# Kernel tuning notes

Measured on AMD Instinct MI355X. Metric: run time of the kernel, lower is better.

## Reference

```python
import jax, jax.numpy as jnp
import numpy as np

N_NODES = 2176
N_IN = 64
N_HID = 2048
N_OUT = 64
NODE_DIM = 64
HEADS = 4


def _build_edge_index():
    hs, os_ = N_IN, N_IN + N_HID
    # input -> hidden block (order: for i: for h)
    s1 = np.repeat(np.arange(0, N_IN), N_HID)
    t1 = np.tile(np.arange(hs, os_), N_IN)
    # hidden -> output block (order: for h: for o)
    s2 = np.repeat(np.arange(hs, os_), N_OUT)
    t2 = np.tile(np.arange(os_, N_NODES), N_HID)
    return jnp.asarray(np.stack([np.concatenate([s1, s2]), np.concatenate([t1, t2])]), dtype=jnp.int32)


def setup_inputs() -> dict:
    key = jax.random.key(0)
    ks = jax.random.split(key, 20)
    D, H = NODE_DIM, HEADS
    edge_index = _build_edge_index()  # [2, E]
    E = edge_index.shape[1]

    def xavier(k, shape):
        fan_in, fan_out = shape[0], shape[1]
        lim = float(np.sqrt(6.0 / (fan_in + fan_out)))
        return jax.random.uniform(k, shape, jnp.float32, -lim, lim)

    return {
        "x_input": jax.random.normal(ks[0], (N_IN,), jnp.float32),
        "node_features": jax.random.normal(ks[1], (N_NODES, D), jnp.float32) * 0.1,
        "edge_weights": jax.random.normal(ks[2], (E, 1), jnp.float32) * 0.1,
        "edge_index": edge_index,
        "wq1": xavier(ks[3], (D, D * H)), "wk1": xavier(ks[4], (D, D * H)),
        "wv1": xavier(ks[5], (D, D * H)), "we1": xavier(ks[6], (1, H)),
        "wo1": xavier(ks[7], (D * H, D)), "bo1": jnp.zeros((D,), jnp.float32),
        "wq2": xavier(ks[8], (D, D * H)), "wk2": xavier(ks[9], (D, D * H)),
        "wv2": xavier(ks[10], (D, D * H)), "we2": xavier(ks[11], (1, H)),
        "wo2": xavier(ks[12], (D * H, D)), "bo2": jnp.zeros((D,), jnp.float32),
        "wproj": xavier(ks[13], (D, 1)), "bproj": jnp.zeros((1,), jnp.float32),
        "num_output_nodes": N_OUT,
    }


def _message_pass(x, edge_index, ew, wq, wk, wv, we, wo, bo):
    # x: [N, D_in]; edge_index: [2, E]; ew: [E, 1]
    src, tgt = edge_index[0], edge_index[1]
    dout = wo.shape[1]
    heads = wq.shape[1] // dout
    q = (x[tgt] @ wq).reshape(-1, heads, dout)  # [E, H, D]
    k = (x[src] @ wk).reshape(-1, heads, dout)
    v = (x[src] @ wv).reshape(-1, heads, dout)
    attn = (q * k).sum(-1) / jnp.sqrt(jnp.float32(dout)) + ew @ we  # [E, H]
    # NOTE: the per-target segment-softmax in the torch source is dead code;
    # the effective math is leaky_relu then a global softmax over edges.
    attn = jax.nn.leaky_relu(attn, negative_slope=0.2)
    attn = jax.nn.softmax(attn, axis=0)
    weighted_v = (attn[:, :, None] * v).reshape(-1, heads * dout)  # [E, H*D]
    out = jax.ops.segment_sum(weighted_v, tgt, num_segments=x.shape[0])  # [N, H*D]
    out = out @ wo + bo
    return out + x  # residual (in_channels == out_channels)


def reference(x_input, node_features, edge_weights, edge_index,
              wq1, wk1, wv1, we1, wo1, bo1,
              wq2, wk2, wv2, we2, wo2, bo2,
              wproj, bproj, num_output_nodes):
    n_in = x_input.shape[0]
    x = node_features.at[:n_in, 0].set(x_input)
    x = jax.nn.relu(_message_pass(x, edge_index, edge_weights, wq1, wk1, wv1, we1, wo1, bo1))
    x = jax.nn.relu(_message_pass(x, edge_index, edge_weights, wq2, wk2, wv2, we2, wo2, bo2))
    out_nodes = x[x.shape[0] - num_output_nodes:]
    output = jax.nn.sigmoid(out_nodes @ wproj + bproj).squeeze()
    return output, x
```

## Files before the change

### kernel.cpp

```cpp
#include <hip/hip_runtime.h>
#include <math.h>

#define E1 131072

__device__ __forceinline__ void gemm_nn_acc(const float* __restrict__ A,
                                            const float* __restrict__ B,
                                            float acc[4][4], int tr, int tc) {
  for (int k4 = 0; k4 < 16; ++k4) {
    float4 b0 = *(const float4*)&B[(k4 * 4 + 0) * 68 + tc * 4];
    float4 b1 = *(const float4*)&B[(k4 * 4 + 1) * 68 + tc * 4];
    float4 b2 = *(const float4*)&B[(k4 * 4 + 2) * 68 + tc * 4];
    float4 b3 = *(const float4*)&B[(k4 * 4 + 3) * 68 + tc * 4];
#pragma unroll
    for (int a = 0; a < 4; ++a) {
      float4 av = *(const float4*)&A[(tr + 16 * a) * 68 + k4 * 4];
      acc[a][0] += av.x * b0.x + av.y * b1.x + av.z * b2.x + av.w * b3.x;
      acc[a][1] += av.x * b0.y + av.y * b1.y + av.z * b2.y + av.w * b3.y;
      acc[a][2] += av.x * b0.z + av.y * b1.z + av.z * b2.z + av.w * b3.z;
      acc[a][3] += av.x * b0.w + av.y * b1.w + av.z * b2.w + av.w * b3.w;
    }
  }
}

__device__ __forceinline__ void gemm_nt_acc(const float* __restrict__ A,
                                            const float* __restrict__ B,
                                            float acc[4][4], int tr, int tc) {
  for (int k4 = 0; k4 < 16; ++k4) {
    float4 av[4], bv[4];
#pragma unroll
    for (int a = 0; a < 4; ++a) av[a] = *(const float4*)&A[(tr + 16 * a) * 68 + k4 * 4];
#pragma unroll
    for (int b = 0; b < 4; ++b) bv[b] = *(const float4*)&B[(tc + 16 * b) * 68 + k4 * 4];
#pragma unroll
    for (int a = 0; a < 4; ++a)
#pragma unroll
      for (int b = 0; b < 4; ++b)
        acc[a][b] += av[a].x * bv[b].x + av[a].y * bv[b].y +
                     av[a].z * bv[b].z + av[a].w * bv[b].w;
  }
}

__device__ __forceinline__ void st_tile(float* __restrict__ C, const float acc[4][4],
                                        int tr, int tc) {
#pragma unroll
  for (int a = 0; a < 4; ++a)
    *(float4*)&C[(tr + 16 * a) * 68 + tc * 4] =
        make_float4(acc[a][0], acc[a][1], acc[a][2], acc[a][3]);
}

__device__ __forceinline__ void ld_x(float* __restrict__ dst, const float* __restrict__ src,
                                     int tid, bool sub, const float* __restrict__ xinp) {
  for (int t4 = tid; t4 < 1024; t4 += 256) {
    int r = t4 >> 4, c0 = (t4 & 15) * 4;
    float4 v = *(const float4*)(src + t4 * 4);
    if (sub && c0 == 0) v.x = xinp[r];
    *(float4*)&dst[r * 68 + c0] = v;
  }
}

__global__ __launch_bounds__(256) void k_mm(const float* __restrict__ wq1, const float* __restrict__ wk1,
                                            const float* __restrict__ wv1, const float* __restrict__ wo1,
                                            const float* __restrict__ wq2, const float* __restrict__ wk2,
                                            const float* __restrict__ wv2, const float* __restrict__ wo2,
                                            float* __restrict__ Mb, float* __restrict__ W2b) {
  __shared__ float A[64 * 68];
  __shared__ float B[64 * 68];
  const int bid = blockIdx.x, tid = threadIdx.x;
  const int L = bid >> 3, type = (bid >> 2) & 1, h = bid & 3;
  const float* wq = L ? wq2 : wq1;
  const float* wk = L ? wk2 : wk1;
  const float* wv = L ? wv2 : wv1;
  const float* wo = L ? wo2 : wo1;
  const int tr = tid >> 4, tc = tid & 15;
  float acc[4][4];
#pragma unroll
  for (int a = 0; a < 4; ++a)
#pragma unroll
    for (int q = 0; q < 4; ++q) acc[a][q] = 0.f;

  if (type == 0) {
    for (int t4 = tid; t4 < 1024; t4 += 256) {
      int r = t4 >> 4, c0 = (t4 & 15) * 4;
      *(float4*)&A[r * 68 + c0] = *(const float4*)(wq + r * 256 + h * 64 + c0);
      *(float4*)&B[r * 68 + c0] = *(const float4*)(wk + r * 256 + h * 64 + c0);
    }
    __syncthreads();
    gemm_nt_acc(A, B, acc, tr, tc);
    float* out = Mb + L * 16384 + h * 4096;
#pragma unroll
    for (int a = 0; a < 4; ++a)
#pragma unroll
      for (int b = 0; b < 4; ++b)
        out[(tr + 16 * a) * 64 + tc + 16 * b] = acc[a][b];
  } else {
    for (int t4 = tid; t4 < 1024; t4 += 256) {
      int r = t4 >> 4, c0 = (t4 & 15) * 4;
      *(float4*)&A[r * 68 + c0] = *(const float4*)(wv + r * 256 + h * 64 + c0);
      *(float4*)&B[r * 68 + c0] = *(const float4*)(wo + (h * 64 + r) * 64 + c0);
    }
    __syncthreads();
    gemm_nn_acc(A, B, acc, tr, tc);
    float* out = W2b + L * 16384;
#pragma unroll
    for (int a = 0; a < 4; ++a)
      *(float4*)&out[(h * 64 + tr + 16 * a) * 64 + tc * 4] =
          make_float4(acc[a][0], acc[a][1], acc[a][2], acc[a][3]);
  }
}

template<bool SUB>
__global__ __launch_bounds__(256) void k_attn(const float* __restrict__ x,
                                              const float* __restrict__ xinp,
                                              const float* __restrict__ Mb,
                                              const float* __restrict__ we,
                                              const float* __restrict__ ew,
                                              float* __restrict__ AggH,
                                              float* __restrict__ part,
                                              float* __restrict__ bsum) {
  __shared__ float A[64 * 68];
  __shared__ float B[64 * 68];
  __shared__ float C[64 * 68];
  __shared__ float D[64 * 68];
  __shared__ float Em[64 * 68];
  __shared__ float wred[4];
  const int bid = blockIdx.x, tid = threadIdx.x;
  const bool r1 = bid < 128;
  const int tile = (r1 ? bid : bid - 128) >> 2;
  const int h = bid & 3;
  const int j0 = tile * 64;
  const int rowSrc = r1 ? 0 : (64 + j0);
  const int rowQ = r1 ? (64 + j0) : 2112;
  const int tr = tid >> 4, tc = tid & 15;
  const float weh = we[h];
  const float* Mh = Mb + h * 4096;

  ld_x(A, x + rowSrc * 64, tid, SUB && r1, xinp);
  ld_x(B, x + rowQ * 64, tid, false, nullptr);
  for (int t4 = tid; t4 < 1024; t4 += 256) {
    int r = t4 >> 4, c0 = (t4 & 15) * 4;
    *(float4*)&Em[r * 68 + c0] = *(const float4*)(Mh + r * 64 + c0);
  }
  if (r1) {
    for (int t4 = tid; t4 < 1024; t4 += 256) {
      int i = t4 >> 4, jl0 = (t4 & 15) * 4;
      *(float4*)&D[i * 68 + jl0] = *(const float4*)(ew + i * 2048 + j0 + jl0);
    }
  } else {
    for (int t4 = tid; t4 < 1024; t4 += 256) {
      int jl = t4 >> 4, o0 = (t4 & 15) * 4;
      *(float4*)&D[jl * 68 + o0] = *(const float4*)(ew + E1 + (j0 + jl) * 64 + o0);
    }
  }
  __syncthreads();

  {
    float t_[4][4];
#pragma unroll
    for (int a = 0; a < 4; ++a)
#pragma unroll
      for (int q = 0; q < 4; ++q) t_[a][q] = 0.f;
    gemm_nn_acc(B, Em, t_, tr, tc);
    st_tile(C, t_, tr, tc);
  }
  __syncthreads();

  float acc[4][4];
#pragma unroll
  for (int a = 0; a < 4; ++a)
#pragma unroll
    for (int b = 0; b < 4; ++b) acc[a][b] = 0.f;
  gemm_nt_acc(C, A, acc, tr, tc);
  float esum = 0.f;
#pragma unroll
  for (int a = 0; a < 4; ++a) {
    int row = tr + 16 * a;
#pragma unroll
    for (int b = 0; b < 4; ++b) {
      int col = tc + 16 * b;
      float v = acc[a][b] * 0.125f + D[col * 68 + row] * weh;
      v = (v >= 0.f) ? v : 0.2f * v;
      v = fminf(v, 60.f);
      float e = __expf(v);
      esum += e;
      B[row * 68 + col] = e;
    }
  }
#pragma unroll
  for (int s = 1; s < 64; s <<= 1) esum += __shfl_xor(esum, s);
  if ((tid & 63) == 0) wred[tid >> 6] = esum;
  __syncthreads();

  float u[4][4];
#pragma unroll
  for (int a = 0; a < 4; ++a)
#pragma unroll
    for (int q = 0; q < 4; ++q) u[a][q] = 0.f;
  gemm_nn_acc(B, A, u, tr, tc);
  if (r1) {
#pragma unroll
    for (int a = 0; a < 4; ++a)
      *(float4*)&AggH[(j0 + tr + 16 * a) * 256 + h * 64 + tc * 4] =
          make_float4(u[a][0], u[a][1], u[a][2], u[a][3]);
  } else {
#pragma unroll
    for (int a = 0; a < 4; ++a)
      *(float4*)&part[tile * 16384 + (tr + 16 * a) * 256 + h * 64 + tc * 4] =
          make_float4(u[a][0], u[a][1], u[a][2], u[a][3]);
  }
  if (tid == 0) bsum[bid] = (wred[0] + wred[1]) + (wred[2] + wred[3]);
}

template<bool SUB, bool HEAD>
__global__ __launch_bounds__(256) void k_proj(const float* __restrict__ xin,
                                              const float* __restrict__ xinp,
                                              const float* __restrict__ AggH,
                                              const float* __restrict__ part,
                                              const float* __restrict__ bsum,
                                              const float* __restrict__ W2,
                                              const float* __restrict__ bo,
                                              const float* __restrict__ wproj,
                                              const float* __restrict__ bproj,
                                              float* __restrict__ xout,
                                              float* __restrict__ outh) {
  __shared__ float As[4][260];
  const int bid = blockIdx.x, tid = threadIdx.x;
  const int n0 = bid * 4;
  const int nl = tid >> 6, d = tid & 63;
  const int node = n0 + nl;

  float inv[4];
  {
    int l = tid & 63;
#pragma unroll
    for (int hh = 0; hh < 4; ++hh) {
      float s = (l < 32) ? bsum[l * 4 + hh] : bsum[128 + (l - 32) * 4 + hh];
#pragma unroll
      for (int st = 1; st < 64; st <<= 1) s += __shfl_xor(s, st);
      inv[hh] = 1.f / s;
    }
  }

  float xres = xin[node * 64 + d];
  if (SUB) {
    if (d == 0 && node < 64) xres = xinp[node];
  }

  float val;
  if (n0 < 64) {
    val = xres + bo[d];
  } else {
    if (n0 < 2112) {
      int a = tid >> 6, c0 = (tid & 63) * 4;
      float4 v = *(const float4*)&AggH[(n0 - 64 + a) * 256 + c0];
      float iv = inv[c0 >> 6];
      *(float4*)&As[a][c0] = make_float4(v.x * iv, v.y * iv, v.z * iv, v.w * iv);
    } else {
      int a = tid >> 6, c0 = (tid & 63) * 4;
      float4 s = make_float4(0.f, 0.f, 0.f, 0.f);
      for (int ch = 0; ch < 32; ++ch) {
        float4 v = *(const float4*)&part[ch * 16384 + (n0 - 2112 + a) * 256 + c0];
        s.x += v.x; s.y += v.y; s.z += v.z; s.w += v.w;
      }
      float iv = inv[c0 >> 6];
      *(float4*)&As[a][c0] = make_float4(s.x * iv, s.y * iv, s.z * iv, s.w * iv);
    }
    __syncthreads();
    float acc = xres + bo[d];
    for (int c4 = 0; c4 < 64; ++c4) {
      float4 a4 = *(const float4*)&As[nl][c4 * 4];
      acc += a4.x * W2[(c4 * 4 + 0) * 64 + d] + a4.y * W2[(c4 * 4 + 1) * 64 + d] +
             a4.z * W2[(c4 * 4 + 2) * 64 + d] + a4.w * W2[(c4 * 4 + 3) * 64 + d];
    }
    val = acc;
  }
  val = fmaxf(val, 0.f);
  xout[node * 64 + d] = val;

  if (HEAD) {
    if (n0 >= 2112) {
      float wv = val * wproj[d];
#pragma unroll
      for (int st = 1; st < 64; st <<= 1) wv += __shfl_xor(wv, st);
      if ((tid & 63) == 0) outh[node - 2112] = 1.f / (1.f + __expf(-(wv + bproj[0])));
    }
  }
}

extern "C" void kernel_launch(void* const* d_in, const int* in_sizes, int n_in,
                              void* d_out, int out_size, void* d_ws, size_t ws_size,
                              hipStream_t stream) {
  const float* x_input       = (const float*)d_in[0];
  const float* node_features = (const float*)d_in[1];
  const float* edge_weights  = (const float*)d_in[2];
  const float* wq1 = (const float*)d_in[4];
  const float* wk1 = (const float*)d_in[5];
  const float* wv1 = (const float*)d_in[6];
  const float* we1 = (const float*)d_in[7];
  const float* wo1 = (const float*)d_in[8];
  const float* bo1 = (const float*)d_in[9];
  const float* wq2 = (const float*)d_in[10];
  const float* wk2 = (const float*)d_in[11];
  const float* wv2 = (const float*)d_in[12];
  const float* we2 = (const float*)d_in[13];
  const float* wo2 = (const float*)d_in[14];
  const float* bo2 = (const float*)d_in[15];
  const float* wproj = (const float*)d_in[16];
  const float* bproj = (const float*)d_in[17];

  float* out = (float*)d_out;
  float* ws = (float*)d_ws;
  float* xB   = ws;
  float* AggH = xB + 139264;
  float* part = AggH + 524288;
  float* bsum = part + 524288;
  float* Mb   = bsum + 256;
  float* W2b  = Mb + 32768;

  k_mm<<<16, 256, 0, stream>>>(wq1, wk1, wv1, wo1, wq2, wk2, wv2, wo2, Mb, W2b);

  k_attn<true><<<256, 256, 0, stream>>>(node_features, x_input, Mb, we1,
                                        edge_weights, AggH, part, bsum);
  k_proj<true, false><<<544, 256, 0, stream>>>(node_features, x_input, AggH, part, bsum,
                                               W2b, bo1, nullptr, nullptr, xB, nullptr);

  k_attn<false><<<256, 256, 0, stream>>>(xB, nullptr, Mb + 16384, we2,
                                         edge_weights, AggH, part, bsum);
  k_proj<false, true><<<544, 256, 0, stream>>>(xB, nullptr, AggH, part, bsum,
                                               W2b + 16384, bo2, wproj, bproj, out + 64, out);
}
```

Baseline: 57.57 us.

## Fold weight-product kernel into first attention kernel, dropping a launch

Removes the separate k_mm launch. The first attention kernel now computes K=x·Wk and Q=x·Wq per head directly instead of using a precomputed Wq·Wk^T matrix. Its first 12 blocks also compute the layer-2 Wq·Wk^T products and both layers' Wv·Wo products for later kernels. This saves a launch and a serial dependency, but adds two extra 64x64 GEMMs per block in layer 1, raises shared memory per block to seven tiles (which may lower occupancy), and gives a few blocks a longer tail.

```diff
diff --git a/kernel.cpp b/kernel.cpp
--- a/kernel.cpp
+++ b/kernel.cpp
@@ -58,70 +58,186 @@
   }
 }
 
-__global__ __launch_bounds__(256) void k_mm(const float* __restrict__ wq1, const float* __restrict__ wk1,
-                                            const float* __restrict__ wv1, const float* __restrict__ wo1,
-                                            const float* __restrict__ wq2, const float* __restrict__ wk2,
-                                            const float* __restrict__ wv2, const float* __restrict__ wo2,
-                                            float* __restrict__ Mb, float* __restrict__ W2b) {
-  __shared__ float A[64 * 68];
-  __shared__ float B[64 * 68];
+__device__ __forceinline__ void ld_w(float* __restrict__ dst, const float* __restrict__ w,
+                                     int h, int tid) {
+  for (int t4 = tid; t4 < 1024; t4 += 256) {
+    int k = t4 >> 4, c0 = (t4 & 15) * 4;
+    *(float4*)&dst[k * 68 + c0] = *(const float4*)(w + k * 256 + h * 64 + c0);
+  }
+}
+
+__global__ __launch_bounds__(256) void k_attn1(const float* __restrict__ x,
+                                               const float* __restrict__ xinp,
+                                               const float* __restrict__ wq1,
+                                               const float* __restrict__ wk1,
+                                               const float* __restrict__ we1,
+                                               const float* __restrict__ ew,
+                                               const float* __restrict__ wq2,
+                                               const float* __restrict__ wk2,
+                                               const float* __restrict__ wv1,
+                                               const float* __restrict__ wo1,
+                                               const float* __restrict__ wv2,
+                                               const float* __restrict__ wo2,
+                                               float* __restrict__ AggH,
+                                               float* __restrict__ part,
+                                               float* __restrict__ bsum,
+                                               float* __restrict__ Mb,
+                                               float* __restrict__ W2b) {
+  __shared__ float A[4352];
+  __shared__ float B[4352];
+  __shared__ float C[4352];
+  __shared__ float D[4352];
+  __shared__ float Ew[4352];
+  __shared__ float F[4352];
+  __shared__ float G[4352];
+  __shared__ float wred[4];
   const int bid = blockIdx.x, tid = threadIdx.x;
-  const int L = bid >> 3, type = (bid >> 2) & 1, h = bid & 3;
-  const float* wq = L ? wq2 : wq1;
-  const float* wk = L ? wk2 : wk1;
-  const float* wv = L ? wv2 : wv1;
-  const float* wo = L ? wo2 : wo1;
+  const bool r1 = bid < 128;
+  const int tile = (r1 ? bid : bid - 128) >> 2;
+  const int h = bid & 3;
+  const int j0 = tile * 64;
+  const int rowSrc = r1 ? 0 : (64 + j0);
+  const int rowQ = r1 ? (64 + j0) : 2112;
   const int tr = tid >> 4, tc = tid & 15;
-  float acc[4][4];
-#pragma unroll
-  for (int a = 0; a < 4; ++a)
-#pragma unroll
-    for (int q = 0; q < 4; ++q) acc[a][q] = 0.f;
-
-  if (type == 0) {
+  const float weh = we1[h];
+
+  ld_x(A, x + rowSrc * 64, tid, r1, xinp);
+  ld_x(B, x + rowQ * 64, tid, false, nullptr);
+  ld_w(Ew, wk1, h, tid);
+  ld_w(F, wq1, h, tid);
+  if (r1) {
     for (int t4 = tid; t4 < 1024; t4 += 256) {
-      int r = t4 >> 4, c0 = (t4 & 15) * 4;
-      *(float4*)&A[r * 68 + c0] = *(const float4*)(wq + r * 256 + h * 64 + c0);
-      *(float4*)&B[r * 68 + c0] = *(const float4*)(wk + r * 256 + h * 64 + c0);
-    }
-    __syncthreads();
-    gemm_nt_acc(A, B, acc, tr, tc);
-    float* out = Mb + L * 16384 + h * 4096;
-#pragma unroll
-    for (int a = 0; a < 4; ++a)
-#pragma unroll
-      for (int b = 0; b < 4; ++b)
-        out[(tr + 16 * a) * 64 + tc + 16 * b] = acc[a][b];
+      int i = t4 >> 4, jl0 = (t4 & 15) * 4;
+      *(float4*)&G[i * 68 + jl0] = *(const float4*)(ew + i * 2048 + j0 + jl0);
+    }
   } else {
     for (int t4 = tid; t4 < 1024; t4 += 256) {
-      int r = t4 >> 4, c0 = (t4 & 15) * 4;
-      *(float4*)&A[r * 68 + c0] = *(const float4*)(wv + r * 256 + h * 64 + c0);
-      *(float4*)&B[r * 68 + c0] = *(const float4*)(wo + (h * 64 + r) * 64 + c0);
-    }
+      int jl = t4 >> 4, o0 = (t4 & 15) * 4;
+      *(float4*)&G[jl * 68 + o0] = *(const float4*)(ew + E1 + (j0 + jl) * 64 + o0);
+    }
+  }
+  __syncthreads();
+
+  {
+    float kt[4][4];
+#pragma unroll
+    for (int a = 0; a < 4; ++a)
+#pragma unroll
+      for (int q = 0; q < 4; ++q) kt[a][q] = 0.f;
+    gemm_nn_acc(A, Ew, kt, tr, tc);
+    st_tile(C, kt, tr, tc);
+    float qt[4][4];
+#pragma unroll
+    for (int a = 0; a < 4; ++a)
+#pragma unroll
+      for (int q = 0; q < 4; ++q) qt[a][q] = 0.f;
+    gemm_nn_acc(B, F, qt, tr, tc);
+    st_tile(D, qt, tr, tc);
+  }
+  __syncthreads();
+
+  float acc[4][4];
+#pragma unroll
+  for (int a = 0; a < 4; ++a)
+#pragma unroll
+    for (int b = 0; b < 4; ++b) acc[a][b] = 0.f;
+  gemm_nt_acc(D, C, acc, tr, tc);
+  float esum = 0.f;
+#pragma unroll
+  for (int a = 0; a < 4; ++a) {
+    int row = tr + 16 * a;
+#pragma unroll
+    for (int b = 0; b < 4; ++b) {
+      int col = tc + 16 * b;
+      float v = acc[a][b] * 0.125f + G[col * 68 + row] * weh;
+      v = (v >= 0.f) ? v : 0.2f * v;
+      v = fminf(v, 60.f);
+      float e = __expf(v);
+      esum += e;
+      B[row * 68 + col] = e;
+    }
+  }
+#pragma unroll
+  for (int s = 1; s < 64; s <<= 1) esum += __shfl_xor(esum, s);
+  if ((tid & 63) == 0) wred[tid >> 6] = esum;
+  __syncthreads();
+
+  float u[4][4];
+#pragma unroll
+  for (int a = 0; a < 4; ++a)
+#pragma unroll
+    for (int q = 0; q < 4; ++q) u[a][q] = 0.f;
+  gemm_nn_acc(B, A, u, tr, tc);
+  if (r1) {
+#pragma unroll
+    for (int a = 0; a < 4; ++a)
+      *(float4*)&AggH[(j0 + tr + 16 * a) * 256 + h * 64 + tc * 4] =
+          make_float4(u[a][0], u[a][1], u[a][2], u[a][3]);
+  } else {
+#pragma unroll
+    for (int a = 0; a < 4; ++a)
+      *(float4*)&part[tile * 16384 + (tr + 16 * a) * 256 + h * 64 + tc * 4] =
+          make_float4(u[a][0], u[a][1], u[a][2], u[a][3]);
+  }
+  if (tid == 0) bsum[bid] = (wred[0] + wred[1]) + (wred[2] + wred[3]);
+
+  if (bid < 12) {
     __syncthreads();
-    gemm_nn_acc(A, B, acc, tr, tc);
-    float* out = W2b + L * 16384;
-#pragma unroll
-    for (int a = 0; a < 4; ++a)
-      *(float4*)&out[(h * 64 + tr + 16 * a) * 64 + tc * 4] =
-          make_float4(acc[a][0], acc[a][1], acc[a][2], acc[a][3]);
-  }
-}
-
-template<bool SUB>
-__global__ __launch_bounds__(256) void k_attn(const float* __restrict__ x,
-                                              const float* __restrict__ xinp,
-                                              const float* __restrict__ Mb,
-                                              const float* __restrict__ we,
-                                              const float* __restrict__ ew,
-                                              float* __restrict__ AggH,
-                                              float* __restrict__ part,
-                                              float* __restrict__ bsum) {
-  __shared__ float A[64 * 68];
-  __shared__ float B[64 * 68];
-  __shared__ float C[64 * 68];
-  __shared__ float D[64 * 68];
-  __shared__ float Em[64 * 68];
+    const int type = bid >> 2, hh = bid & 3;
+    if (type == 0) {
+      for (int t4 = tid; t4 < 1024; t4 += 256) {
+        int r = t4 >> 4, c0 = (t4 & 15) * 4;
+        *(float4*)&A[r * 68 + c0] = *(const float4*)(wq2 + r * 256 + hh * 64 + c0);
+        *(float4*)&B[r * 68 + c0] = *(const float4*)(wk2 + r * 256 + hh * 64 + c0);
+      }
+      __syncthreads();
+      float m[4][4];
+#pragma unroll
+      for (int a = 0; a < 4; ++a)
+#pragma unroll
+        for (int b = 0; b < 4; ++b) m[a][b] = 0.f;
+      gemm_nt_acc(A, B, m, tr, tc);
+#pragma unroll
+      for (int a = 0; a < 4; ++a)
+#pragma unroll
+        for (int b = 0; b < 4; ++b)
+          Mb[hh * 4096 + (tr + 16 * a) * 64 + tc + 16 * b] = m[a][b];
+    } else {
+      const float* wv = (type == 1) ? wv1 : wv2;
+      const float* wo = (type == 1) ? wo1 : wo2;
+      for (int t4 = tid; t4 < 1024; t4 += 256) {
+        int r = t4 >> 4, c0 = (t4 & 15) * 4;
+        *(float4*)&A[r * 68 + c0] = *(const float4*)(wv + r * 256 + hh * 64 + c0);
+        *(float4*)&B[r * 68 + c0] = *(const float4*)(wo + (hh * 64 + r) * 64 + c0);
+      }
+      __syncthreads();
+      float m[4][4];
+#pragma unroll
+      for (int a = 0; a < 4; ++a)
+#pragma unroll
+        for (int b = 0; b < 4; ++b) m[a][b] = 0.f;
+      gemm_nn_acc(A, B, m, tr, tc);
+      float* o = W2b + (type - 1) * 16384;
+#pragma unroll
+      for (int a = 0; a < 4; ++a)
+        *(float4*)&o[(hh * 64 + tr + 16 * a) * 64 + tc * 4] =
+            make_float4(m[a][0], m[a][1], m[a][2], m[a][3]);
+    }
+  }
+}
+
+__global__ __launch_bounds__(256) void k_attn2(const float* __restrict__ x,
+                                               const float* __restrict__ Mb,
+                                               const float* __restrict__ we,
+                                               const float* __restrict__ ew,
+                                               float* __restrict__ AggH,
+                                               float* __restrict__ part,
+                                               float* __restrict__ bsum) {
+  __shared__ float A[4352];
+  __shared__ float B[4352];
+  __shared__ float C[4352];
+  __shared__ float D[4352];
+  __shared__ float Em[4352];
   __shared__ float wred[4];
   const int bid = blockIdx.x, tid = threadIdx.x;
   const bool r1 = bid < 128;
@@ -134,7 +250,7 @@
   const float weh = we[h];
   const float* Mh = Mb + h * 4096;
 
-  ld_x(A, x + rowSrc * 64, tid, SUB && r1, xinp);
+  ld_x(A, x + rowSrc * 64, tid, false, nullptr);
   ld_x(B, x + rowQ * 64, tid, false, nullptr);
   for (int t4 = tid; t4 < 1024; t4 += 256) {
     int r = t4 >> 4, c0 = (t4 & 15) * 4;
@@ -314,17 +430,14 @@
   float* part = AggH + 524288;
   float* bsum = part + 524288;
   float* Mb   = bsum + 256;
-  float* W2b  = Mb + 32768;
-
-  k_mm<<<16, 256, 0, stream>>>(wq1, wk1, wv1, wo1, wq2, wk2, wv2, wo2, Mb, W2b);
-
-  k_attn<true><<<256, 256, 0, stream>>>(node_features, x_input, Mb, we1,
-                                        edge_weights, AggH, part, bsum);
+  float* W2b  = Mb + 16384;
+
+  k_attn1<<<256, 256, 0, stream>>>(node_features, x_input, wq1, wk1, we1, edge_weights,
+                                   wq2, wk2, wv1, wo1, wv2, wo2,
+                                   AggH, part, bsum, Mb, W2b);
   k_proj<true, false><<<544, 256, 0, stream>>>(node_features, x_input, AggH, part, bsum,
                                                W2b, bo1, nullptr, nullptr, xB, nullptr);
-
-  k_attn<false><<<256, 256, 0, stream>>>(xB, nullptr, Mb + 16384, we2,
-                                         edge_weights, AggH, part, bsum);
+  k_attn2<<<256, 256, 0, stream>>>(xB, Mb, we2, edge_weights, AggH, part, bsum);
   k_proj<false, true><<<544, 256, 0, stream>>>(xB, nullptr, AggH, part, bsum,
                                                W2b + 16384, bo2, wproj, bproj, out + 64, out);
 }
```

Measured after the change: 58.15 us. No clear change (+1.0%).
